# Kernel optimization log

Hardware: AMD Instinct MI355X
Metric: run time of the kernel (lower is better)

Reference implementation:

```python
import jax, jax.numpy as jnp
import numpy as np

INPUT_DIM = 1024
HIDDEN = 2048
N_QUBITS = 16
N_LAYERS = 6
BATCH = 16384


def setup_inputs() -> dict:
    key = jax.random.key(0)
    ks = jax.random.split(key, 8)
    x = jax.random.normal(ks[0], (BATCH, INPUT_DIM), dtype=jnp.float32)
    # encoder: Linear(input_dim, hidden) -> ReLU -> Linear(hidden, n_qubits) -> Tanh
    W1 = jax.random.normal(ks[1], (INPUT_DIM, HIDDEN), dtype=jnp.float32) / np.sqrt(INPUT_DIM)
    b1 = jnp.zeros((HIDDEN,), dtype=jnp.float32)
    W2 = jax.random.normal(ks[2], (HIDDEN, N_QUBITS), dtype=jnp.float32) / np.sqrt(HIDDEN)
    b2 = jnp.zeros((N_QUBITS,), dtype=jnp.float32)
    vqc_params = jax.random.normal(ks[3], (N_LAYERS, N_QUBITS, 2), dtype=jnp.float32) * 0.1
    Wd = jax.random.normal(ks[4], (N_QUBITS, 1), dtype=jnp.float32) / np.sqrt(N_QUBITS)
    bd = jnp.zeros((1,), dtype=jnp.float32)
    return {"x": x, "W1": W1, "b1": b1, "W2": W2, "b2": b2,
            "vqc_params": vqc_params, "Wd": Wd, "bd": bd}


def reference(x, W1, b1, W2, b2, vqc_params, Wd, bd):
    # classical encoder
    h = jax.nn.relu(x @ W1 + b1)
    encoded = jnp.tanh(h @ W2 + b2)          # [B, Q]
    # variational quantum circuit (vectorized over qubits)
    state = jnp.sin(encoded * jnp.pi)
    for layer in range(N_LAYERS):
        theta = vqc_params[layer, :, 0]      # [Q]
        phi = vqc_params[layer, :, 1]        # [Q]
        state = jnp.cos(theta) * state + jnp.sin(theta) * jnp.cos(phi)
        if layer < N_LAYERS - 1:
            # pairwise entanglement: target <- 0.1*control + 0.9*target for pairs (2i, 2i+1)
            state = state.at[:, 1::2].set(state[:, 0::2] * 0.1 + state[:, 1::2] * 0.9)
    out = jax.nn.sigmoid(state @ Wd + bd)    # [B, 1]
    return out
```

## Files before the change

### kernel.cpp

```cpp
#include <hip/hip_runtime.h>

typedef unsigned short u16;
typedef unsigned int u32;
typedef float f32x4 __attribute__((ext_vector_type(4)));
typedef short bf16x8 __attribute__((ext_vector_type(8)));

#define AS1 __attribute__((address_space(1)))
#define AS3 __attribute__((address_space(3)))

__device__ __forceinline__ void g2l16(const void* g, void* l) {
  __builtin_amdgcn_global_load_lds((const AS1 void*)g, (AS3 void*)l, 16, 0, 0);
}

__device__ __forceinline__ u32 bfr(float f) {
  u32 u = __float_as_uint(f);
  return (u + 0x7fffu + ((u >> 16) & 1u)) >> 16;
}

#define PI_F 3.14159265358979323846f

__global__ __launch_bounds__(256) void cvt_x(const float* __restrict__ x, u16* __restrict__ xb) {
  long t = (long)blockIdx.x * blockDim.x + threadIdx.x;
  const float4 a = ((const float4*)x)[t * 2 + 0];
  const float4 b = ((const float4*)x)[t * 2 + 1];
  uint4 o;
  o.x = bfr(a.x) | (bfr(a.y) << 16);
  o.y = bfr(a.z) | (bfr(a.w) << 16);
  o.z = bfr(b.x) | (bfr(b.y) << 16);
  o.w = bfr(b.z) | (bfr(b.w) << 16);
  ((uint4*)xb)[t] = o;
}

__global__ __launch_bounds__(256) void cvt_w1t(const float* __restrict__ W1, u16* __restrict__ w1t) {
  __shared__ u16 T[64][65];
  int bid = blockIdx.x;
  int kt = (bid & 15) << 6;
  int nt = (bid >> 4) << 6;
  int tid = threadIdx.x;
  #pragma unroll
  for (int i = 0; i < 16; ++i) {
    int e = i * 256 + tid;
    int r = e >> 6, c = e & 63;
    T[r][c] = (u16)bfr(W1[(long)(kt + r) * 2048 + nt + c]);
  }
  __syncthreads();
  #pragma unroll
  for (int i = 0; i < 16; ++i) {
    int e = i * 256 + tid;
    int n = e >> 6, k = e & 63;
    w1t[(long)(nt + n) * 1024 + kt + k] = T[k][n];
  }
}

__global__ __launch_bounds__(256) void cvt_w2t(const float* __restrict__ W2, u16* __restrict__ w2t) {
  int idx = blockIdx.x * 256 + threadIdx.x;
  int k = idx >> 4, q = idx & 15;
  w2t[q * 2048 + k] = (u16)bfr(W2[idx]);
}

__global__ __launch_bounds__(512, 2) void gemm1_fused(
    const u16* __restrict__ xb, const u16* __restrict__ w1t,
    const float* __restrict__ b1, const u16* __restrict__ w2t,
    float* __restrict__ Ep) {
  __shared__ __align__(16) char LDS[131072];
  char* const lA0 = LDS;
  char* const lA1 = LDS + 32768;
  char* const lB0 = LDS + 65536;
  char* const lB1 = LDS + 98304;

  const int bswz = (blockIdx.x & 7) * 64 + (blockIdx.x >> 3);
  const int tm = bswz >> 3;
  const int tn = bswz & 7;
  const int tid = threadIdx.x;
  const int lane = tid & 63;
  const int wid = tid >> 6;
  const int wm = wid >> 2;
  const int wn = wid & 3;
  const int l15 = lane & 15;
  const int cg = lane >> 4;
  const int key = (l15 & 7) << 4;
  const int cb0 = (cg * 16) ^ key;
  const int cb1 = (64 + cg * 16) ^ key;

  const u16* Ag = xb + (long)tm * 256 * 1024;
  const u16* Bg = w1t + (long)tn * 256 * 1024;

  bf16x8 a[4][2];
  bf16x8 b[2][2][2];
  f32x4 acc[8][4] = {};

#define STGA(sl, t, h) do {                                                  \
    _Pragma("unroll")                                                        \
    for (int rr = 0; rr < 2; ++rr) {                                         \
      int off = rr * 8192 + tid * 16;                                        \
      int rh = off >> 7;                                                     \
      int r = ((rh >> 6) << 7) + (h) * 64 + (rh & 63);                       \
      int cb = (off & 127) ^ ((r & 7) << 4);                                 \
      g2l16((const char*)Ag + (long)r * 2048 + (t) * 128 + cb,               \
            (sl) + (h) * 16384 + off);                                       \
    } } while (0)

#define STGB(sl, t, h) do {                                                  \
    _Pragma("unroll")                                                        \
    for (int rr = 0; rr < 2; ++rr) {                                         \
      int off = rr * 8192 + tid * 16;                                        \
      int rh = off >> 7;                                                     \
      int r = ((rh >> 5) << 6) + (h) * 32 + (rh & 31);                       \
      int cb = (off & 127) ^ ((r & 7) << 4);                                 \
      g2l16((const char*)Bg + (long)r * 2048 + (t) * 128 + cb,               \
            (sl) + (h) * 16384 + off);                                       \
    } } while (0)

#define RDA(sl, mh) do {                                                     \
    _Pragma("unroll")                                                        \
    for (int m = 0; m < 4; ++m) {                                            \
      int ro = (wm * 64 + m * 16 + l15) * 128 + (mh) * 16384;                \
      a[m][0] = *(const bf16x8*)((sl) + ro + cb0);                           \
      a[m][1] = *(const bf16x8*)((sl) + ro + cb1);                           \
    } } while (0)

#define RDB(sl, nh) do {                                                     \
    _Pragma("unroll")                                                        \
    for (int n = 0; n < 2; ++n) {                                            \
      int ro = (wn * 32 + n * 16 + l15) * 128 + (nh) * 16384;                \
      b[nh][n][0] = *(const bf16x8*)((sl) + ro + cb0);                       \
      b[nh][n][1] = *(const bf16x8*)((sl) + ro + cb1);                       \
    } } while (0)

#define MM2(mh) do {                                                         \
    __builtin_amdgcn_s_setprio(1);                                           \
    _Pragma("unroll")                                                        \
    for (int m = 0; m < 4; ++m)                                              \
      _Pragma("unroll")                                                      \
      for (int nh = 0; nh < 2; ++nh)                                         \
        _Pragma("unroll")                                                    \
        for (int n = 0; n < 2; ++n) {                                        \
          acc[(mh)*4+m][nh*2+n] = __builtin_amdgcn_mfma_f32_16x16x32_bf16(   \
              a[m][0], b[nh][n][0], acc[(mh)*4+m][nh*2+n], 0, 0, 0);         \
          acc[(mh)*4+m][nh*2+n] = __builtin_amdgcn_mfma_f32_16x16x32_bf16(   \
              a[m][1], b[nh][n][1], acc[(mh)*4+m][nh*2+n], 0, 0, 0);         \
        }                                                                    \
    __builtin_amdgcn_s_setprio(0);                                           \
  } while (0)

#define SB  __builtin_amdgcn_sched_barrier(0)
#define BAR __builtin_amdgcn_s_barrier()
#define GATE(n) do { SB;                                                     \
    asm volatile("s_waitcnt vmcnt(" #n ")" ::: "memory");                    \
    BAR; SB; } while (0)

  STGA(lA0, 0, 0); STGB(lB0, 0, 0); STGB(lB0, 0, 1);
  STGA(lA0, 0, 1);
  STGA(lA1, 1, 0); STGB(lB1, 1, 0); STGB(lB1, 1, 1);
  GATE(8);

  #pragma unroll 1
  for (int j = 0; j < 8; ++j) {
    const int ta2 = 2 * j + 2, tb2 = 2 * j + 3;
    const bool pf = (j < 7);
    STGA(lA1, 2 * j + 1, 1);
    RDA(lA0, 0); RDB(lB0, 0); RDB(lB0, 1);
    MM2(0);
    GATE(8);
    if (pf) { STGA(lA0, ta2, 0); STGB(lB0, ta2, 0); STGB(lB0, ta2, 1); }
    RDA(lA0, 1);
    MM2(1);
    if (pf) GATE(8); else GATE(2);
    if (pf) STGA(lA0, ta2, 1);
    RDA(lA1, 0); RDB(lB1, 0); RDB(lB1, 1);
    MM2(0);
    if (pf) GATE(8); else GATE(0);
    if (pf) { STGA(lA1, tb2, 0); STGB(lB1, tb2, 0); STGB(lB1, tb2, 1); }
    RDA(lA1, 1);
    MM2(1);
    if (pf) GATE(8); else GATE(0);
  }

  char* Pw = LDS + wid * 16384;
  #pragma unroll
  for (int n = 0; n < 4; ++n) {
    const float bias = b1[tn * 256 + wn * 64 + n * 16 + l15];
    #pragma unroll
    for (int mr = 0; mr < 8; ++mr) {
      #pragma unroll
      for (int jj = 0; jj < 4; ++jj) {
        int row = mr * 16 + cg * 4 + jj;
        float v = acc[mr][n][jj] + bias;
        v = v > 0.f ? v : 0.f;
        int cbyte = ((n * 16 + l15) * 2) ^ ((row & 7) << 4);
        *(u16*)(Pw + row * 128 + cbyte) = (u16)bfr(v);
      }
    }
  }
  const u16* w2p = w2t + l15 * 2048 + tn * 256 + wn * 64;
  bf16x8 bw0 = *(const bf16x8*)(w2p + cg * 8);
  bf16x8 bw1 = *(const bf16x8*)(w2p + 32 + cg * 8);
  f32x4 acc2[8];
  #pragma unroll
  for (int mf = 0; mf < 8; ++mf) {
    bf16x8 a0 = *(const bf16x8*)(Pw + (mf * 16 + l15) * 128 + ((cg * 16) ^ key));
    bf16x8 a1 = *(const bf16x8*)(Pw + (mf * 16 + l15) * 128 + ((64 + cg * 16) ^ key));
    f32x4 z = {0.f, 0.f, 0.f, 0.f};
    z = __builtin_amdgcn_mfma_f32_16x16x32_bf16(a0, bw0, z, 0, 0, 0);
    z = __builtin_amdgcn_mfma_f32_16x16x32_bf16(a1, bw1, z, 0, 0, 0);
    acc2[mf] = z;
  }
  __syncthreads();
  float* Ew = (float*)LDS;
  #pragma unroll
  for (int mf = 0; mf < 8; ++mf)
    #pragma unroll
    for (int rg = 0; rg < 4; ++rg)
      Ew[(wm * 128 + mf * 16 + cg * 4 + rg) * 68 + l15 * 4 + wn] = acc2[mf][rg];
  __syncthreads();
  #pragma unroll
  for (int c = tid; c < 4096; c += 512) {
    int wmh = c >> 11, row = (c >> 4) & 127, q = c & 15;
    const float* e4 = &Ew[(wmh * 128 + row) * 68 + q * 4];
    float s = e4[0] + e4[1] + e4[2] + e4[3];
    Ep[(long)tn * (16384 * 16) + (long)(tm * 256 + wmh * 128 + row) * 16 + q] = s;
  }
#undef STGA
#undef STGB
#undef RDA
#undef RDB
#undef MM2
#undef SB
#undef BAR
#undef GATE
}

__global__ __launch_bounds__(256) void vqc_final(
    const float* __restrict__ Ep, const float* __restrict__ b2,
    const float* __restrict__ vqc, const float* __restrict__ Wd,
    const float* __restrict__ bd, float* __restrict__ out) {
  const int tid = threadIdx.x;
  const int lane = tid & 63;
  const int wave = tid >> 6;
  const int q = lane & 15;
  const int g = lane >> 4;
  const int row = blockIdx.x * 16 + wave * 4 + g;

  float e = 0.f;
  #pragma unroll
  for (int p = 0; p < 8; ++p)
    e += Ep[(long)p * (16384 * 16) + (long)row * 16 + q];

  float ct[6], sp[6];
  #pragma unroll
  for (int L = 0; L < 6; ++L) {
    float th = vqc[(L * 16 + q) * 2 + 0];
    float ph = vqc[(L * 16 + q) * 2 + 1];
    ct[L] = __cosf(th);
    sp[L] = __sinf(th) * __cosf(ph);
  }
  float s = __sinf(tanhf(e + b2[q]) * PI_F);
  #pragma unroll
  for (int L = 0; L < 6; ++L) {
    s = ct[L] * s + sp[L];
    if (L < 5) {
      float ps = __shfl_xor(s, 1, 64);
      s = (q & 1) ? (0.1f * ps + 0.9f * s) : s;
    }
  }
  float p = s * Wd[q];
  p += __shfl_xor(p, 1, 64);
  p += __shfl_xor(p, 2, 64);
  p += __shfl_xor(p, 4, 64);
  p += __shfl_xor(p, 8, 64);
  if (q == 0) out[row] = 1.f / (1.f + __expf(-(p + bd[0])));
}

__global__ __launch_bounds__(256) void fallback(
    const float* __restrict__ x, const float* __restrict__ W1,
    const float* __restrict__ b1, const float* __restrict__ W2,
    const float* __restrict__ b2, const float* __restrict__ vqc,
    const float* __restrict__ Wd, const float* __restrict__ bd,
    float* __restrict__ out) {
  __shared__ float xs[4][1024];
  __shared__ float E[4][16];
  const int bid = blockIdx.x;
  const int tid = threadIdx.x;
  const int r0 = bid * 4;
  for (int i = tid; i < 4 * 1024; i += 256)
    xs[i >> 10][i & 1023] = x[(long)(r0 + (i >> 10)) * 1024 + (i & 1023)];
  if (tid < 64) ((float*)E)[tid] = 0.f;
  __syncthreads();
  float pE[4][16];
  #pragma unroll
  for (int r = 0; r < 4; ++r)
    #pragma unroll
    for (int qq = 0; qq < 16; ++qq) pE[r][qq] = 0.f;
  for (int jj = 0; jj < 8; ++jj) {
    int j = jj * 256 + tid;
    float h0 = 0, h1 = 0, h2 = 0, h3 = 0;
    for (int k = 0; k < 1024; ++k) {
      float w = W1[(long)k * 2048 + j];
      h0 += xs[0][k] * w; h1 += xs[1][k] * w; h2 += xs[2][k] * w; h3 += xs[3][k] * w;
    }
    float hh[4] = {h0, h1, h2, h3};
    #pragma unroll
    for (int r = 0; r < 4; ++r) {
      float hr = hh[r] + b1[j];
      hr = hr > 0.f ? hr : 0.f;
      #pragma unroll
      for (int qq = 0; qq < 16; ++qq) pE[r][qq] += hr * W2[j * 16 + qq];
    }
  }
  #pragma unroll
  for (int r = 0; r < 4; ++r)
    #pragma unroll
    for (int qq = 0; qq < 16; ++qq) atomicAdd(&E[r][qq], pE[r][qq]);
  __syncthreads();
  if (tid < 4) {
    int r = tid;
    float s[16];
    #pragma unroll
    for (int qq = 0; qq < 16; ++qq)
      s[qq] = __sinf(tanhf(E[r][qq] + b2[qq]) * PI_F);
    #pragma unroll
    for (int L = 0; L < 6; ++L) {
      #pragma unroll
      for (int qq = 0; qq < 16; ++qq)
        s[qq] = __cosf(vqc[(L * 16 + qq) * 2]) * s[qq] +
                __sinf(vqc[(L * 16 + qq) * 2]) * __cosf(vqc[(L * 16 + qq) * 2 + 1]);
      if (L < 5)
        #pragma unroll
        for (int qq = 1; qq < 16; qq += 2) s[qq] = 0.1f * s[qq - 1] + 0.9f * s[qq];
    }
    float z = bd[0];
    #pragma unroll
    for (int qq = 0; qq < 16; ++qq) z += s[qq] * Wd[qq];
    out[r0 + r] = 1.f / (1.f + __expf(-z));
  }
}

extern "C" void kernel_launch(void* const* d_in, const int* in_sizes, int n_in,
                              void* d_out, int out_size, void* d_ws, size_t ws_size,
                              hipStream_t stream) {
  const float* x   = (const float*)d_in[0];
  const float* W1  = (const float*)d_in[1];
  const float* b1  = (const float*)d_in[2];
  const float* W2  = (const float*)d_in[3];
  const float* b2  = (const float*)d_in[4];
  const float* vqc = (const float*)d_in[5];
  const float* Wd  = (const float*)d_in[6];
  const float* bd  = (const float*)d_in[7];
  float* out = (float*)d_out;

  const size_t OFF_XB  = 0;
  const size_t OFF_W1T = 33554432;
  const size_t OFF_W2T = 37748736;
  const size_t OFF_EP  = 37814272;
  const size_t NEED    = 46202880;

  if (ws_size < NEED) {
    fallback<<<4096, 256, 0, stream>>>(x, W1, b1, W2, b2, vqc, Wd, bd, out);
    return;
  }
  u16*   xb  = (u16*)((char*)d_ws + OFF_XB);
  u16*   w1t = (u16*)((char*)d_ws + OFF_W1T);
  u16*   w2t = (u16*)((char*)d_ws + OFF_W2T);
  float* Ep  = (float*)((char*)d_ws + OFF_EP);

  cvt_x<<<8192, 256, 0, stream>>>(x, xb);
  cvt_w1t<<<512, 256, 0, stream>>>(W1, w1t);
  cvt_w2t<<<128, 256, 0, stream>>>(W2, w2t);
  gemm1_fused<<<512, 512, 0, stream>>>(xb, w1t, b1, w2t, Ep);
  vqc_final<<<1024, 256, 0, stream>>>(Ep, b2, vqc, Wd, bd, out);
}
```

Measured before the change: 91.95 us.

## Retile fused GEMM to 128x256 blocks with triple-buffered K=32 pipeline

Shrinks the GEMM1 block tile from 256x256 with 8 waves to 128x256 with 4 waves, doubling the grid to 1024 blocks. The K loop moves from double-buffered 64-wide steps to a three-stage ring of 32-wide steps with a new XOR swizzle, cutting LDS to 72KB so two blocks fit per CU. The block-to-tile mapping is also changed so each XCD owns a contiguous range of M tiles. Each A tile now feeds fewer MFMAs, so data reuse drops, and there are more barriers per unit of work.

After: 102.4 us. 1.11x slower.

```diff
diff --git a/kernel.cpp b/kernel.cpp
--- a/kernel.cpp
+++ b/kernel.cpp
@@ -58,88 +58,75 @@
   w2t[q * 2048 + k] = (u16)bfr(W2[idx]);
 }
 
-__global__ __launch_bounds__(512, 2) void gemm1_fused(
+__global__ __launch_bounds__(256, 2) void gemm1_fused(
     const u16* __restrict__ xb, const u16* __restrict__ w1t,
     const float* __restrict__ b1, const u16* __restrict__ w2t,
     float* __restrict__ Ep) {
-  __shared__ __align__(16) char LDS[131072];
-  char* const lA0 = LDS;
-  char* const lA1 = LDS + 32768;
-  char* const lB0 = LDS + 65536;
-  char* const lB1 = LDS + 98304;
-
-  const int bswz = (blockIdx.x & 7) * 64 + (blockIdx.x >> 3);
-  const int tm = bswz >> 3;
-  const int tn = bswz & 7;
+  __shared__ __align__(16) char LDS[73728];
+
+  const int xcd = blockIdx.x & 7;
+  const int idx = blockIdx.x >> 3;
+  const int tm = xcd * 16 + (idx >> 3);
+  const int tn = idx & 7;
   const int tid = threadIdx.x;
   const int lane = tid & 63;
-  const int wid = tid >> 6;
-  const int wm = wid >> 2;
-  const int wn = wid & 3;
+  const int wn = tid >> 6;
   const int l15 = lane & 15;
   const int cg = lane >> 4;
-  const int key = (l15 & 7) << 4;
-  const int cb0 = (cg * 16) ^ key;
-  const int cb1 = (64 + cg * 16) ^ key;
-
-  const u16* Ag = xb + (long)tm * 256 * 1024;
+  const int rk = ((l15 >> 1) & 3) << 4;
+  const int cbr = (cg << 4) ^ rk;
+  const int pkey = (l15 & 7) << 4;
+
+  const u16* Ag = xb + (long)tm * 128 * 1024;
   const u16* Bg = w1t + (long)tn * 256 * 1024;
 
-  bf16x8 a[4][2];
-  bf16x8 b[2][2][2];
+  char* s0 = LDS;
+  char* s1 = LDS + 24576;
+  char* s2 = LDS + 49152;
+
+  bf16x8 a[8], b[4];
   f32x4 acc[8][4] = {};
 
-#define STGA(sl, t, h) do {                                                  \
+#define STGA(sl, t) do {                                                     \
     _Pragma("unroll")                                                        \
     for (int rr = 0; rr < 2; ++rr) {                                         \
-      int off = rr * 8192 + tid * 16;                                        \
-      int rh = off >> 7;                                                     \
-      int r = ((rh >> 6) << 7) + (h) * 64 + (rh & 63);                       \
-      int cb = (off & 127) ^ ((r & 7) << 4);                                 \
-      g2l16((const char*)Ag + (long)r * 2048 + (t) * 128 + cb,               \
-            (sl) + (h) * 16384 + off);                                       \
+      int off = rr * 4096 + tid * 16;                                        \
+      int row = off >> 6;                                                    \
+      int ch = (off >> 4) & 3;                                               \
+      int cb = ((ch ^ ((row >> 1) & 3)) << 4);                               \
+      g2l16((const char*)Ag + (long)row * 2048 + (t) * 64 + cb,              \
+            (sl) + off);                                                     \
     } } while (0)
 
-#define STGB(sl, t, h) do {                                                  \
-    _Pragma("unroll")                                                        \
-    for (int rr = 0; rr < 2; ++rr) {                                         \
-      int off = rr * 8192 + tid * 16;                                        \
-      int rh = off >> 7;                                                     \
-      int r = ((rh >> 5) << 6) + (h) * 32 + (rh & 31);                       \
-      int cb = (off & 127) ^ ((r & 7) << 4);                                 \
-      g2l16((const char*)Bg + (long)r * 2048 + (t) * 128 + cb,               \
-            (sl) + (h) * 16384 + off);                                       \
+#define STGB(sl, t) do {                                                     \
+    _Pragma("unroll")                                                        \
+    for (int rr = 0; rr < 4; ++rr) {                                         \
+      int off = rr * 4096 + tid * 16;                                        \
+      int row = off >> 6;                                                    \
+      int ch = (off >> 4) & 3;                                               \
+      int cb = ((ch ^ ((row >> 1) & 3)) << 4);                               \
+      g2l16((const char*)Bg + (long)row * 2048 + (t) * 64 + cb,              \
+            (sl) + 8192 + off);                                              \
     } } while (0)
 
-#define RDA(sl, mh) do {                                                     \
-    _Pragma("unroll")                                                        \
-    for (int m = 0; m < 4; ++m) {                                            \
-      int ro = (wm * 64 + m * 16 + l15) * 128 + (mh) * 16384;                \
-      a[m][0] = *(const bf16x8*)((sl) + ro + cb0);                           \
-      a[m][1] = *(const bf16x8*)((sl) + ro + cb1);                           \
-    } } while (0)
-
-#define RDB(sl, nh) do {                                                     \
-    _Pragma("unroll")                                                        \
-    for (int n = 0; n < 2; ++n) {                                            \
-      int ro = (wn * 32 + n * 16 + l15) * 128 + (nh) * 16384;                \
-      b[nh][n][0] = *(const bf16x8*)((sl) + ro + cb0);                       \
-      b[nh][n][1] = *(const bf16x8*)((sl) + ro + cb1);                       \
-    } } while (0)
-
-#define MM2(mh) do {                                                         \
+#define RDALL(sl) do {                                                       \
+    _Pragma("unroll")                                                        \
+    for (int m = 0; m < 8; ++m)                                              \
+      a[m] = *(const bf16x8*)((sl) + m * 1024 + l15 * 64 + cbr);             \
+    _Pragma("unroll")                                                        \
+    for (int n = 0; n < 4; ++n)                                              \
+      b[n] = *(const bf16x8*)((sl) + 8192 + wn * 4096 + n * 1024 +           \
+                              l15 * 64 + cbr);                               \
+  } while (0)
+
+#define MM32() do {                                                          \
     __builtin_amdgcn_s_setprio(1);                                           \
     _Pragma("unroll")                                                        \
-    for (int m = 0; m < 4; ++m)                                              \
+    for (int m = 0; m < 8; ++m)                                              \
       _Pragma("unroll")                                                      \
-      for (int nh = 0; nh < 2; ++nh)                                         \
-        _Pragma("unroll")                                                    \
-        for (int n = 0; n < 2; ++n) {                                        \
-          acc[(mh)*4+m][nh*2+n] = __builtin_amdgcn_mfma_f32_16x16x32_bf16(   \
-              a[m][0], b[nh][n][0], acc[(mh)*4+m][nh*2+n], 0, 0, 0);         \
-          acc[(mh)*4+m][nh*2+n] = __builtin_amdgcn_mfma_f32_16x16x32_bf16(   \
-              a[m][1], b[nh][n][1], acc[(mh)*4+m][nh*2+n], 0, 0, 0);         \
-        }                                                                    \
+      for (int n = 0; n < 4; ++n)                                            \
+        acc[m][n] = __builtin_amdgcn_mfma_f32_16x16x32_bf16(                 \
+            a[m], b[n], acc[m][n], 0, 0, 0);                                 \
     __builtin_amdgcn_s_setprio(0);                                           \
   } while (0)
 
@@ -149,34 +136,23 @@
     asm volatile("s_waitcnt vmcnt(" #n ")" ::: "memory");                    \
     BAR; SB; } while (0)
 
-  STGA(lA0, 0, 0); STGB(lB0, 0, 0); STGB(lB0, 0, 1);
-  STGA(lA0, 0, 1);
-  STGA(lA1, 1, 0); STGB(lB1, 1, 0); STGB(lB1, 1, 1);
-  GATE(8);
+  STGA(s0, 0); STGB(s0, 0);
+  STGA(s1, 1); STGB(s1, 1);
+  GATE(6);
 
   #pragma unroll 1
-  for (int j = 0; j < 8; ++j) {
-    const int ta2 = 2 * j + 2, tb2 = 2 * j + 3;
-    const bool pf = (j < 7);
-    STGA(lA1, 2 * j + 1, 1);
-    RDA(lA0, 0); RDB(lB0, 0); RDB(lB0, 1);
-    MM2(0);
-    GATE(8);
-    if (pf) { STGA(lA0, ta2, 0); STGB(lB0, ta2, 0); STGB(lB0, ta2, 1); }
-    RDA(lA0, 1);
-    MM2(1);
-    if (pf) GATE(8); else GATE(2);
-    if (pf) STGA(lA0, ta2, 1);
-    RDA(lA1, 0); RDB(lB1, 0); RDB(lB1, 1);
-    MM2(0);
-    if (pf) GATE(8); else GATE(0);
-    if (pf) { STGA(lA1, tb2, 0); STGB(lB1, tb2, 0); STGB(lB1, tb2, 1); }
-    RDA(lA1, 1);
-    MM2(1);
-    if (pf) GATE(8); else GATE(0);
-  }
-
-  char* Pw = LDS + wid * 16384;
+  for (int j = 0; j < 32; ++j) {
+    const bool pf = (j < 30);
+    if (pf) { STGA(s2, j + 2); STGB(s2, j + 2); }
+    RDALL(s0);
+    MM32();
+    if (pf)            GATE(6);
+    else if (j == 30)  GATE(0);
+    char* rot = s0; s0 = s1; s1 = s2; s2 = rot;
+  }
+  __syncthreads();
+
+  char* Pw = LDS + wn * 16384;
   #pragma unroll
   for (int n = 0; n < 4; ++n) {
     const float bias = b1[tn * 256 + wn * 64 + n * 16 + l15];
@@ -198,8 +174,8 @@
   f32x4 acc2[8];
   #pragma unroll
   for (int mf = 0; mf < 8; ++mf) {
-    bf16x8 a0 = *(const bf16x8*)(Pw + (mf * 16 + l15) * 128 + ((cg * 16) ^ key));
-    bf16x8 a1 = *(const bf16x8*)(Pw + (mf * 16 + l15) * 128 + ((64 + cg * 16) ^ key));
+    bf16x8 a0 = *(const bf16x8*)(Pw + (mf * 16 + l15) * 128 + ((cg * 16) ^ pkey));
+    bf16x8 a1 = *(const bf16x8*)(Pw + (mf * 16 + l15) * 128 + ((64 + cg * 16) ^ pkey));
     f32x4 z = {0.f, 0.f, 0.f, 0.f};
     z = __builtin_amdgcn_mfma_f32_16x16x32_bf16(a0, bw0, z, 0, 0, 0);
     z = __builtin_amdgcn_mfma_f32_16x16x32_bf16(a1, bw1, z, 0, 0, 0);
@@ -211,20 +187,19 @@
   for (int mf = 0; mf < 8; ++mf)
     #pragma unroll
     for (int rg = 0; rg < 4; ++rg)
-      Ew[(wm * 128 + mf * 16 + cg * 4 + rg) * 68 + l15 * 4 + wn] = acc2[mf][rg];
-  __syncthreads();
-  #pragma unroll
-  for (int c = tid; c < 4096; c += 512) {
-    int wmh = c >> 11, row = (c >> 4) & 127, q = c & 15;
-    const float* e4 = &Ew[(wmh * 128 + row) * 68 + q * 4];
+      Ew[(mf * 16 + cg * 4 + rg) * 68 + l15 * 4 + wn] = acc2[mf][rg];
+  __syncthreads();
+  #pragma unroll
+  for (int c = tid; c < 2048; c += 256) {
+    int row = c >> 4, q = c & 15;
+    const float* e4 = &Ew[row * 68 + q * 4];
     float s = e4[0] + e4[1] + e4[2] + e4[3];
-    Ep[(long)tn * (16384 * 16) + (long)(tm * 256 + wmh * 128 + row) * 16 + q] = s;
+    Ep[(long)tn * (16384 * 16) + (long)(tm * 128 + row) * 16 + q] = s;
   }
 #undef STGA
 #undef STGB
-#undef RDA
-#undef RDB
-#undef MM2
+#undef RDALL
+#undef MM32
 #undef SB
 #undef BAR
 #undef GATE
@@ -366,6 +341,6 @@
   cvt_x<<<8192, 256, 0, stream>>>(x, xb);
   cvt_w1t<<<512, 256, 0, stream>>>(W1, w1t);
   cvt_w2t<<<128, 256, 0, stream>>>(W2, w2t);
-  gemm1_fused<<<512, 512, 0, stream>>>(xb, w1t, b1, w2t, Ep);
+  gemm1_fused<<<1024, 256, 0, stream>>>(xb, w1t, b1, w2t, Ep);
   vqc_final<<<1024, 256, 0, stream>>>(Ep, b2, vqc, Wd, bd, out);
 }
```

## Load W1 operand directly from global into registers, staging only A in LDS

Applied to the files above, without the earlier changes.

The B (W1^T) operand of the fused GEMM is no longer staged in LDS. Each wave now loads its own 64-column slice straight from global memory into double-buffered registers. Only the A tile goes through LDS, and the pipeline is simplified to two half-steps per iteration, each followed by a full vmcnt(0) wait and barrier. This removes LDS traffic and bank pressure for B, at the cost of more vector registers, redundant global loads of B across the two wm waves, and coarser waits that may expose memory latency.

After: 127.0 us. 1.38x slower.

```diff
diff --git a/kernel.cpp b/kernel.cpp
--- a/kernel.cpp
+++ b/kernel.cpp
@@ -65,8 +65,6 @@
   __shared__ __align__(16) char LDS[131072];
   char* const lA0 = LDS;
   char* const lA1 = LDS + 32768;
-  char* const lB0 = LDS + 65536;
-  char* const lB1 = LDS + 98304;
 
   const int bswz = (blockIdx.x & 7) * 64 + (blockIdx.x >> 3);
   const int tm = bswz >> 3;
@@ -83,98 +81,75 @@
   const int cb1 = (64 + cg * 16) ^ key;
 
   const u16* Ag = xb + (long)tm * 256 * 1024;
-  const u16* Bg = w1t + (long)tn * 256 * 1024;
+  const u16* bptr = w1t + (long)(tn * 256 + wn * 64 + l15) * 1024 + cg * 8;
 
   bf16x8 a[4][2];
-  bf16x8 b[2][2][2];
+  bf16x8 bA[4][2], bB[4][2];
   f32x4 acc[8][4] = {};
 
-#define STGA(sl, t, h) do {                                                  \
+#define STGA(sl, t) do {                                                     \
     _Pragma("unroll")                                                        \
-    for (int rr = 0; rr < 2; ++rr) {                                         \
-      int off = rr * 8192 + tid * 16;                                        \
-      int rh = off >> 7;                                                     \
-      int r = ((rh >> 6) << 7) + (h) * 64 + (rh & 63);                       \
-      int cb = (off & 127) ^ ((r & 7) << 4);                                 \
-      g2l16((const char*)Ag + (long)r * 2048 + (t) * 128 + cb,               \
-            (sl) + (h) * 16384 + off);                                       \
+    for (int i = 0; i < 4; ++i) {                                            \
+      int off = i * 8192 + tid * 16;                                         \
+      int row = off >> 7;                                                    \
+      int cb = (off & 127) ^ ((row & 7) << 4);                               \
+      g2l16((const char*)Ag + (long)row * 2048 + (t) * 128 + cb,             \
+            (sl) + off);                                                     \
     } } while (0)
 
-#define STGB(sl, t, h) do {                                                  \
+#define LDB(dst, t) do {                                                     \
     _Pragma("unroll")                                                        \
-    for (int rr = 0; rr < 2; ++rr) {                                         \
-      int off = rr * 8192 + tid * 16;                                        \
-      int rh = off >> 7;                                                     \
-      int r = ((rh >> 5) << 6) + (h) * 32 + (rh & 31);                       \
-      int cb = (off & 127) ^ ((r & 7) << 4);                                 \
-      g2l16((const char*)Bg + (long)r * 2048 + (t) * 128 + cb,               \
-            (sl) + (h) * 16384 + off);                                       \
-    } } while (0)
+    for (int n = 0; n < 4; ++n)                                              \
+      _Pragma("unroll")                                                      \
+      for (int kk = 0; kk < 2; ++kk)                                         \
+        dst[n][kk] = *(const bf16x8*)(bptr + n * 16384 + (t) * 64 + kk * 32);\
+  } while (0)
 
 #define RDA(sl, mh) do {                                                     \
     _Pragma("unroll")                                                        \
     for (int m = 0; m < 4; ++m) {                                            \
-      int ro = (wm * 64 + m * 16 + l15) * 128 + (mh) * 16384;                \
+      int ro = (wm * 128 + (mh) * 64 + m * 16 + l15) * 128;                  \
       a[m][0] = *(const bf16x8*)((sl) + ro + cb0);                           \
       a[m][1] = *(const bf16x8*)((sl) + ro + cb1);                           \
     } } while (0)
 
-#define RDB(sl, nh) do {                                                     \
-    _Pragma("unroll")                                                        \
-    for (int n = 0; n < 2; ++n) {                                            \
-      int ro = (wn * 32 + n * 16 + l15) * 128 + (nh) * 16384;                \
-      b[nh][n][0] = *(const bf16x8*)((sl) + ro + cb0);                       \
-      b[nh][n][1] = *(const bf16x8*)((sl) + ro + cb1);                       \
-    } } while (0)
-
-#define MM2(mh) do {                                                         \
+#define MMh(mh, bX) do {                                                     \
     __builtin_amdgcn_s_setprio(1);                                           \
     _Pragma("unroll")                                                        \
     for (int m = 0; m < 4; ++m)                                              \
       _Pragma("unroll")                                                      \
-      for (int nh = 0; nh < 2; ++nh)                                         \
-        _Pragma("unroll")                                                    \
-        for (int n = 0; n < 2; ++n) {                                        \
-          acc[(mh)*4+m][nh*2+n] = __builtin_amdgcn_mfma_f32_16x16x32_bf16(   \
-              a[m][0], b[nh][n][0], acc[(mh)*4+m][nh*2+n], 0, 0, 0);         \
-          acc[(mh)*4+m][nh*2+n] = __builtin_amdgcn_mfma_f32_16x16x32_bf16(   \
-              a[m][1], b[nh][n][1], acc[(mh)*4+m][nh*2+n], 0, 0, 0);         \
-        }                                                                    \
+      for (int n = 0; n < 4; ++n) {                                          \
+        acc[(mh)*4+m][n] = __builtin_amdgcn_mfma_f32_16x16x32_bf16(          \
+            a[m][0], bX[n][0], acc[(mh)*4+m][n], 0, 0, 0);                   \
+        acc[(mh)*4+m][n] = __builtin_amdgcn_mfma_f32_16x16x32_bf16(          \
+            a[m][1], bX[n][1], acc[(mh)*4+m][n], 0, 0, 0);                   \
+      }                                                                      \
     __builtin_amdgcn_s_setprio(0);                                           \
   } while (0)
 
 #define SB  __builtin_amdgcn_sched_barrier(0)
 #define BAR __builtin_amdgcn_s_barrier()
-#define GATE(n) do { SB;                                                     \
-    asm volatile("s_waitcnt vmcnt(" #n ")" ::: "memory");                    \
+#define GATE0 do { SB;                                                       \
+    asm volatile("s_waitcnt vmcnt(0)" ::: "memory");                         \
     BAR; SB; } while (0)
 
-  STGA(lA0, 0, 0); STGB(lB0, 0, 0); STGB(lB0, 0, 1);
-  STGA(lA0, 0, 1);
-  STGA(lA1, 1, 0); STGB(lB1, 1, 0); STGB(lB1, 1, 1);
-  GATE(8);
+  STGA(lA0, 0);
+  LDB(bA, 0);
+  GATE0;
 
   #pragma unroll 1
   for (int j = 0; j < 8; ++j) {
-    const int ta2 = 2 * j + 2, tb2 = 2 * j + 3;
-    const bool pf = (j < 7);
-    STGA(lA1, 2 * j + 1, 1);
-    RDA(lA0, 0); RDB(lB0, 0); RDB(lB0, 1);
-    MM2(0);
-    GATE(8);
-    if (pf) { STGA(lA0, ta2, 0); STGB(lB0, ta2, 0); STGB(lB0, ta2, 1); }
-    RDA(lA0, 1);
-    MM2(1);
-    if (pf) GATE(8); else GATE(2);
-    if (pf) STGA(lA0, ta2, 1);
-    RDA(lA1, 0); RDB(lB1, 0); RDB(lB1, 1);
-    MM2(0);
-    if (pf) GATE(8); else GATE(0);
-    if (pf) { STGA(lA1, tb2, 0); STGB(lB1, tb2, 0); STGB(lB1, tb2, 1); }
-    RDA(lA1, 1);
-    MM2(1);
-    if (pf) GATE(8); else GATE(0);
-  }
+    STGA(lA1, 2 * j + 1);
+    LDB(bB, 2 * j + 1);
+    RDA(lA0, 0); MMh(0, bA);
+    RDA(lA0, 1); MMh(1, bA);
+    GATE0;
+    if (j < 7) { STGA(lA0, 2 * j + 2); LDB(bA, 2 * j + 2); }
+    RDA(lA1, 0); MMh(0, bB);
+    RDA(lA1, 1); MMh(1, bB);
+    GATE0;
+  }
+  __syncthreads();
 
   char* Pw = LDS + wid * 16384;
   #pragma unroll
@@ -221,13 +196,12 @@
     Ep[(long)tn * (16384 * 16) + (long)(tm * 256 + wmh * 128 + row) * 16 + q] = s;
   }
 #undef STGA
-#undef STGB
+#undef LDB
 #undef RDA
-#undef RDB
-#undef MM2
+#undef MMh
 #undef SB
 #undef BAR
-#undef GATE
+#undef GATE0
 }
 
 __global__ __launch_bounds__(256) void vqc_final(
```

## Switch GEMM to 32x32x16 MFMA and merge conversion kernels into one launch

Applied to the files above, without the earlier changes.

The main GEMM's inner product moves from 16x16x32 bf16 MFMA tiles to 32x32x16 tiles. LDS fragment reads, accumulator layout and the bias/ReLU epilogue are reworked to match. The larger tiles cut the number of LDS fragment loads per FLOP and the instruction count. Separately, the three fp32-to-bf16 conversion kernels are merged into one launch, which removes two launch gaps. The new epilogue row mapping must match the 32x32 accumulator layout exactly or results will be wrong.

Result: slower. 95.32 us (+3.7%).

```diff
diff --git a/kernel.cpp b/kernel.cpp
--- a/kernel.cpp
+++ b/kernel.cpp
@@ -3,6 +3,7 @@
 typedef unsigned short u16;
 typedef unsigned int u32;
 typedef float f32x4 __attribute__((ext_vector_type(4)));
+typedef float f32x16 __attribute__((ext_vector_type(16)));
 typedef short bf16x8 __attribute__((ext_vector_type(8)));
 
 #define AS1 __attribute__((address_space(1)))
@@ -19,24 +20,28 @@
 
 #define PI_F 3.14159265358979323846f
 
-__global__ __launch_bounds__(256) void cvt_x(const float* __restrict__ x, u16* __restrict__ xb) {
-  long t = (long)blockIdx.x * blockDim.x + threadIdx.x;
-  const float4 a = ((const float4*)x)[t * 2 + 0];
-  const float4 b = ((const float4*)x)[t * 2 + 1];
-  uint4 o;
-  o.x = bfr(a.x) | (bfr(a.y) << 16);
-  o.y = bfr(a.z) | (bfr(a.w) << 16);
-  o.z = bfr(b.x) | (bfr(b.y) << 16);
-  o.w = bfr(b.z) | (bfr(b.w) << 16);
-  ((uint4*)xb)[t] = o;
-}
-
-__global__ __launch_bounds__(256) void cvt_w1t(const float* __restrict__ W1, u16* __restrict__ w1t) {
+__global__ __launch_bounds__(256) void cvt_all(
+    const float* __restrict__ x, const float* __restrict__ W1,
+    const float* __restrict__ W2, u16* __restrict__ xb,
+    u16* __restrict__ w1t, u16* __restrict__ w2t) {
   __shared__ u16 T[64][65];
+  const int tid = threadIdx.x;
   int bid = blockIdx.x;
+  if (bid < 8192) {
+    long t = (long)bid * 256 + tid;
+    const float4 a = ((const float4*)x)[t * 2 + 0];
+    const float4 b = ((const float4*)x)[t * 2 + 1];
+    uint4 o;
+    o.x = bfr(a.x) | (bfr(a.y) << 16);
+    o.y = bfr(a.z) | (bfr(a.w) << 16);
+    o.z = bfr(b.x) | (bfr(b.y) << 16);
+    o.w = bfr(b.z) | (bfr(b.w) << 16);
+    ((uint4*)xb)[t] = o;
+    return;
+  }
+  bid -= 8192;
   int kt = (bid & 15) << 6;
   int nt = (bid >> 4) << 6;
-  int tid = threadIdx.x;
   #pragma unroll
   for (int i = 0; i < 16; ++i) {
     int e = i * 256 + tid;
@@ -50,12 +55,11 @@
     int n = e >> 6, k = e & 63;
     w1t[(long)(nt + n) * 1024 + kt + k] = T[k][n];
   }
-}
-
-__global__ __launch_bounds__(256) void cvt_w2t(const float* __restrict__ W2, u16* __restrict__ w2t) {
-  int idx = blockIdx.x * 256 + threadIdx.x;
-  int k = idx >> 4, q = idx & 15;
-  w2t[q * 2048 + k] = (u16)bfr(W2[idx]);
+  if (bid < 128) {
+    int idx = bid * 256 + tid;
+    int k = idx >> 4, q = idx & 15;
+    w2t[q * 2048 + k] = (u16)bfr(W2[idx]);
+  }
 }
 
 __global__ __launch_bounds__(512, 2) void gemm1_fused(
@@ -78,16 +82,17 @@
   const int wn = wid & 3;
   const int l15 = lane & 15;
   const int cg = lane >> 4;
+  const int l31 = lane & 31;
+  const int hi = lane >> 5;
   const int key = (l15 & 7) << 4;
-  const int cb0 = (cg * 16) ^ key;
-  const int cb1 = (64 + cg * 16) ^ key;
+  const int key32 = (l31 & 7) << 4;
 
   const u16* Ag = xb + (long)tm * 256 * 1024;
   const u16* Bg = w1t + (long)tn * 256 * 1024;
 
-  bf16x8 a[4][2];
-  bf16x8 b[2][2][2];
-  f32x4 acc[8][4] = {};
+  bf16x8 a[2][4];
+  bf16x8 b[2][4];
+  f32x16 acc[4][2] = {};
 
 #define STGA(sl, t, h) do {                                                  \
     _Pragma("unroll")                                                        \
@@ -113,33 +118,32 @@
 
 #define RDA(sl, mh) do {                                                     \
     _Pragma("unroll")                                                        \
-    for (int m = 0; m < 4; ++m) {                                            \
-      int ro = (wm * 64 + m * 16 + l15) * 128 + (mh) * 16384;                \
-      a[m][0] = *(const bf16x8*)((sl) + ro + cb0);                           \
-      a[m][1] = *(const bf16x8*)((sl) + ro + cb1);                           \
+    for (int mf = 0; mf < 2; ++mf) {                                         \
+      int ro = (wm * 64 + mf * 32 + l31) * 128 + (mh) * 16384;               \
+      _Pragma("unroll")                                                      \
+      for (int ks = 0; ks < 4; ++ks)                                         \
+        a[mf][ks] = *(const bf16x8*)((sl) + ro +                             \
+                                     ((ks * 32 + hi * 16) ^ key32));         \
     } } while (0)
 
 #define RDB(sl, nh) do {                                                     \
-    _Pragma("unroll")                                                        \
-    for (int n = 0; n < 2; ++n) {                                            \
-      int ro = (wn * 32 + n * 16 + l15) * 128 + (nh) * 16384;                \
-      b[nh][n][0] = *(const bf16x8*)((sl) + ro + cb0);                       \
-      b[nh][n][1] = *(const bf16x8*)((sl) + ro + cb1);                       \
-    } } while (0)
+    int ro = (wn * 32 + l31) * 128 + (nh) * 16384;                           \
+    _Pragma("unroll")                                                        \
+    for (int ks = 0; ks < 4; ++ks)                                           \
+      b[nh][ks] = *(const bf16x8*)((sl) + ro +                               \
+                                   ((ks * 32 + hi * 16) ^ key32));           \
+  } while (0)
 
 #define MM2(mh) do {                                                         \
     __builtin_amdgcn_s_setprio(1);                                           \
     _Pragma("unroll")                                                        \
-    for (int m = 0; m < 4; ++m)                                              \
+    for (int mf = 0; mf < 2; ++mf)                                           \
       _Pragma("unroll")                                                      \
       for (int nh = 0; nh < 2; ++nh)                                         \
         _Pragma("unroll")                                                    \
-        for (int n = 0; n < 2; ++n) {                                        \
-          acc[(mh)*4+m][nh*2+n] = __builtin_amdgcn_mfma_f32_16x16x32_bf16(   \
-              a[m][0], b[nh][n][0], acc[(mh)*4+m][nh*2+n], 0, 0, 0);         \
-          acc[(mh)*4+m][nh*2+n] = __builtin_amdgcn_mfma_f32_16x16x32_bf16(   \
-              a[m][1], b[nh][n][1], acc[(mh)*4+m][nh*2+n], 0, 0, 0);         \
-        }                                                                    \
+        for (int ks = 0; ks < 4; ++ks)                                       \
+          acc[(mh)*2+mf][nh] = __builtin_amdgcn_mfma_f32_32x32x16_bf16(      \
+              a[mf][ks], b[nh][ks], acc[(mh)*2+mf][nh], 0, 0, 0);            \
     __builtin_amdgcn_s_setprio(0);                                           \
   } while (0)
 
@@ -178,17 +182,17 @@
 
   char* Pw = LDS + wid * 16384;
   #pragma unroll
-  for (int n = 0; n < 4; ++n) {
-    const float bias = b1[tn * 256 + wn * 64 + n * 16 + l15];
-    #pragma unroll
-    for (int mr = 0; mr < 8; ++mr) {
+  for (int nh = 0; nh < 2; ++nh) {
+    const float bias = b1[tn * 256 + wn * 64 + nh * 32 + l31];
+    const int colb = (nh * 32 + l31) * 2;
+    #pragma unroll
+    for (int f = 0; f < 4; ++f) {
       #pragma unroll
-      for (int jj = 0; jj < 4; ++jj) {
-        int row = mr * 16 + cg * 4 + jj;
-        float v = acc[mr][n][jj] + bias;
+      for (int reg = 0; reg < 16; ++reg) {
+        int row = f * 32 + (reg & 3) + 8 * (reg >> 2) + 4 * hi;
+        float v = acc[f][nh][reg] + bias;
         v = v > 0.f ? v : 0.f;
-        int cbyte = ((n * 16 + l15) * 2) ^ ((row & 7) << 4);
-        *(u16*)(Pw + row * 128 + cbyte) = (u16)bfr(v);
+        *(u16*)(Pw + row * 128 + (colb ^ ((row & 7) << 4))) = (u16)bfr(v);
       }
     }
   }
@@ -363,9 +367,7 @@
   u16*   w2t = (u16*)((char*)d_ws + OFF_W2T);
   float* Ep  = (float*)((char*)d_ws + OFF_EP);
 
-  cvt_x<<<8192, 256, 0, stream>>>(x, xb);
-  cvt_w1t<<<512, 256, 0, stream>>>(W1, w1t);
-  cvt_w2t<<<128, 256, 0, stream>>>(W2, w2t);
+  cvt_all<<<8704, 256, 0, stream>>>(x, W1, W2, xb, w1t, w2t);
   gemm1_fused<<<512, 512, 0, stream>>>(xb, w1t, b1, w2t, Ep);
   vqc_final<<<1024, 256, 0, stream>>>(Ep, b2, vqc, Wd, bd, out);
 }
```
